# Kernel tuning notes

Hardware: AMD Instinct MI355X
Metric: run time of the kernel (lower is better)

The kernel has to match this reference:

```python
import jax, jax.numpy as jnp
import numpy as np

BETA1 = 0.9
BETA2 = 0.8
THRESH = 1.0  # snntorch Leaky default threshold

T, B, NI, NH, NO = 100, 1024, 256, 512, 10


def setup_inputs() -> dict:
    key = jax.random.key(0)
    kx, k1, k2 = jax.random.split(key, 3)
    x = jax.random.normal(kx, (T, B, NI), dtype=jnp.float32)
    # Weight_synapse 'bin_random_prob' init: binary {0, w} with given probs
    W1 = (jax.random.uniform(k1, (NH, NI)) < 0.8).astype(jnp.float32) * 0.5
    W2 = (jax.random.uniform(k2, (NO, NH)) < 0.5).astype(jnp.float32) * 0.5
    return {"x": x, "W1": W1, "W2": W2}


def _lif(mem, cur, beta):
    # snntorch Leaky, reset_mechanism='subtract': reset from previous mem,
    # then mem = beta*mem + cur - reset*threshold; spk = heaviside(mem - thr)
    reset = (mem > THRESH).astype(cur.dtype)
    mem = beta * mem + cur - reset * THRESH
    spk = (mem > THRESH).astype(cur.dtype)
    return spk, mem


def reference(x, W1, W2):
    b = x.shape[1]
    mem1_0 = jnp.zeros((b, W1.shape[0]), x.dtype)
    mem2_0 = jnp.zeros((b, W2.shape[0]), x.dtype)

    def step(carry, xt):
        mem1, mem2 = carry
        cur1 = xt @ W1.T                      # [B, NH]
        spk1, mem1 = _lif(mem1, cur1, BETA1)
        cur2 = spk1 @ W2.T                    # [B, NO]
        spk2, mem2 = _lif(mem2, cur2, BETA2)
        return (mem1, mem2), (cur1, cur2, spk1, spk2, mem1, mem2)

    _, (cur1, cur2, spk1, spk2, mem1, mem2) = jax.lax.scan(step, (mem1_0, mem2_0), x)
    # matches {'cur':[c1,c2],'spks':[s1,s2],'mem':[m1,m2]}, each stacked on time
    return cur1, cur2, spk1, spk2, mem1, mem2
```

## Files before the change

kernel.cpp:

```cpp
#include <hip/hip_runtime.h>

#define TT 100
#define BB 1024
#define NI 256
#define NH 512
#define NO 10
#define TB (TT*BB)
#define GK 512
#define GN 512

constexpr long long C1_OFF = 0;
constexpr long long C2_OFF = 52428800LL;
constexpr long long S1_OFF = 53452800LL;
constexpr long long S2_OFF = 105881600LL;
constexpr long long M1_OFF = 106905600LL;
constexpr long long M2_OFF = 159334400LL;

typedef short bf16x8 __attribute__((ext_vector_type(8)));
typedef float f32x4 __attribute__((ext_vector_type(4)));

__device__ __forceinline__ unsigned int rne_bf16(float f) {
    unsigned int u = __float_as_uint(f);
    return (u + 0x7fffu + ((u >> 16) & 1u)) >> 16;
}

__device__ __forceinline__ unsigned int pack_hilo(float f) {
    unsigned int hi = rne_bf16(f);
    float hif = __uint_as_float(hi << 16);
    float e = f - hif;
    unsigned int lo = rne_bf16(e);
    return (hi & 0xffffu) | (lo << 16);
}

__global__ void prep_w_kernel(const float* __restrict__ W1, short* __restrict__ Wp) {
    int i = blockIdx.x * blockDim.x + threadIdx.x;
    if (i >= NH * NI / 4) return;
    float4 v = ((const float4*)W1)[i];
    float f[4] = {v.x, v.y, v.z, v.w};
    uint4 o;
    unsigned int* op = &o.x;
    #pragma unroll
    for (int j = 0; j < 4; ++j) {
        unsigned int hb = __float_as_uint(f[j]) >> 16;
        op[j] = hb | (hb << 16);
    }
    ((uint4*)Wp)[i] = o;
}

__launch_bounds__(256, 2)
__global__ void gemm1_kernel(const float* __restrict__ x, const short* __restrict__ Wp,
                             float* __restrict__ C) {
    __shared__ short As[128][40];
    __shared__ short Ws[128][40];
    const int tid = threadIdx.x;
    const int bid = blockIdx.x;
    const int m0 = (bid >> 2) * 128;
    const int n0 = (bid & 3) * 128;
    const int wid = tid >> 6;
    const int lane = tid & 63;
    const int wm = (wid >> 1) * 64;
    const int wn = (wid & 1) * 64;

    f32x4 acc[4][4] = {};

    const int srow = tid >> 2;
    const int sc4 = tid & 3;
    const long long ax0 = (long long)(m0 + srow) * NI + sc4 * 4;
    const long long ax1 = ax0 + 64LL * NI;
    const long long wr0 = (long long)(n0 + srow) * GK + sc4 * 8;
    const long long wr1 = wr0 + 64LL * GK;

    const int fr = lane & 15;
    const int fk = (lane >> 4) * 8;

    float4 a0 = *(const float4*)&x[ax0];
    float4 a1 = *(const float4*)&x[ax1];
    uint4 w0 = *(const uint4*)&Wp[wr0];
    uint4 w1 = *(const uint4*)&Wp[wr1];
    uint4 pa0, pa1;
    pa0.x = pack_hilo(a0.x); pa0.y = pack_hilo(a0.y); pa0.z = pack_hilo(a0.z); pa0.w = pack_hilo(a0.w);
    pa1.x = pack_hilo(a1.x); pa1.y = pack_hilo(a1.y); pa1.z = pack_hilo(a1.z); pa1.w = pack_hilo(a1.w);

    for (int kt = 0; kt < GK / 32; ++kt) {
        __syncthreads();
        *(uint4*)&As[srow][sc4 * 8]      = pa0;
        *(uint4*)&As[srow + 64][sc4 * 8] = pa1;
        *(uint4*)&Ws[srow][sc4 * 8]      = w0;
        *(uint4*)&Ws[srow + 64][sc4 * 8] = w1;
        __syncthreads();

        const int ktn = (kt + 1 < GK / 32) ? kt + 1 : kt;
        a0 = *(const float4*)&x[ax0 + (long long)ktn * 16];
        a1 = *(const float4*)&x[ax1 + (long long)ktn * 16];
        w0 = *(const uint4*)&Wp[wr0 + (long long)ktn * 32];
        w1 = *(const uint4*)&Wp[wr1 + (long long)ktn * 32];
        pa0.x = pack_hilo(a0.x); pa0.y = pack_hilo(a0.y); pa0.z = pack_hilo(a0.z); pa0.w = pack_hilo(a0.w);
        pa1.x = pack_hilo(a1.x); pa1.y = pack_hilo(a1.y); pa1.z = pack_hilo(a1.z); pa1.w = pack_hilo(a1.w);

        bf16x8 af[4], wf[4];
        #pragma unroll
        for (int i = 0; i < 4; ++i) {
            af[i] = *(const bf16x8*)&As[wm + i * 16 + fr][fk];
            wf[i] = *(const bf16x8*)&Ws[wn + i * 16 + fr][fk];
        }
        #pragma unroll
        for (int i = 0; i < 4; ++i)
            #pragma unroll
            for (int j = 0; j < 4; ++j)
                acc[i][j] = __builtin_amdgcn_mfma_f32_16x16x32_bf16(af[i], wf[j], acc[i][j], 0, 0, 0);
    }

    const int col = lane & 15;
    const int rbase = (lane >> 4) * 4;
    #pragma unroll
    for (int i = 0; i < 4; ++i) {
        #pragma unroll
        for (int j = 0; j < 4; ++j) {
            long long base = (long long)(m0 + wm + i * 16 + rbase) * GN + (n0 + wn + j * 16 + col);
            #pragma unroll
            for (int r = 0; r < 4; ++r)
                C[base + (long long)r * GN] = acc[i][j][r];
        }
    }
}

__launch_bounds__(512)
__global__ void lif_kernel(const float* __restrict__ cur1, const float* __restrict__ W2,
                           float* __restrict__ out) {
    const int b = blockIdx.x;
    const int h = threadIdx.x;
    const int w = h >> 6;
    const int lane = h & 63;

    __shared__ unsigned long long wmks[2][8];
    __shared__ unsigned long long w2ms[NO][8];

    #pragma unroll
    for (int o = 0; o < NO; ++o) {
        unsigned long long mk = __ballot(W2[o * NH + h] != 0.0f);
        if (lane == 0) w2ms[o][w] = mk;
    }
    __syncthreads();
    unsigned long long w2m[8];
    if (h < NO) {
        #pragma unroll
        for (int i = 0; i < 8; ++i) w2m[i] = w2ms[h][i];
    }

    float m1 = 0.0f, m2 = 0.0f;
    const long long idx1 = (long long)b * NH + h;
    const float* c1p = cur1 + idx1;
    float* s1p = out + S1_OFF + idx1;
    float* m1p = out + M1_OFF + idx1;
    const long long st1 = (long long)BB * NH;

    for (int t = 0; t < TT; ++t) {
        float c1 = c1p[(long long)t * st1];
        float rst = (m1 > 1.0f) ? 1.0f : 0.0f;
        m1 = 0.9f * m1 + c1 - rst;
        float s1 = (m1 > 1.0f) ? 1.0f : 0.0f;
        s1p[(long long)t * st1] = s1;
        m1p[(long long)t * st1] = m1;

        unsigned long long mk = __ballot(s1 != 0.0f);
        if (lane == 0) wmks[t & 1][w] = mk;
        __syncthreads();

        if (h < NO) {
            int cnt = 0;
            #pragma unroll
            for (int i = 0; i < 8; ++i) cnt += __popcll(wmks[t & 1][i] & w2m[i]);
            float c2 = 0.5f * (float)cnt;
            float rst2 = (m2 > 1.0f) ? 1.0f : 0.0f;
            m2 = 0.8f * m2 + c2 - rst2;
            float s2 = (m2 > 1.0f) ? 1.0f : 0.0f;
            long long o2 = (long long)t * (BB * NO) + b * NO + h;
            out[C2_OFF + o2] = c2;
            out[S2_OFF + o2] = s2;
            out[M2_OFF + o2] = m2;
        }
    }
}

extern "C" void kernel_launch(void* const* d_in, const int* in_sizes, int n_in,
                              void* d_out, int out_size, void* d_ws, size_t ws_size,
                              hipStream_t stream) {
    const float* x  = (const float*)d_in[0];
    const float* W1 = (const float*)d_in[1];
    const float* W2 = (const float*)d_in[2];
    float* out = (float*)d_out;

    short* Wp = (short*)(out + S1_OFF);
    float* C1 = out + C1_OFF;

    {
        int w4 = NH * NI / 4;
        prep_w_kernel<<<(w4 + 255) / 256, 256, 0, stream>>>(W1, Wp);
    }
    {
        gemm1_kernel<<<(TB / 128) * (GN / 128), 256, 0, stream>>>(x, Wp, C1);
    }
    lif_kernel<<<BB, NH, 0, stream>>>(C1, W2, out);
}
```

Before: 261.8 us.

## Chunk time into two GEMM+LIF passes, async LDS weight loads with swizzled pre-tiled layout

Splits the time axis into two chunks so each gemm1 launch writes a smaller cur1 slab that the following lif pass reads while it may still be cache-resident. The LIF state is carried between chunks by reading back the last stored mem values. W1 is pre-tiled into a swizzled image and streamed into a double-buffered LDS tile with global_load_lds, removing register staging and bank conflicts. The LIF loop also prefetches the next cur1 value. This adds launches and a serial dependency between chunks, and it relocates the weight scratch inside the output buffer.

```diff
diff --git a/kernel.cpp b/kernel.cpp
--- a/kernel.cpp
+++ b/kernel.cpp
@@ -8,6 +8,7 @@
 #define TB (TT*BB)
 #define GK 512
 #define GN 512
+#define TCH 50
 
 constexpr long long C1_OFF = 0;
 constexpr long long C2_OFF = 52428800LL;
@@ -32,11 +33,27 @@
     return (hi & 0xffffu) | (lo << 16);
 }
 
-__global__ void prep_w_kernel(const float* __restrict__ W1, short* __restrict__ Wp) {
+__device__ __forceinline__ void pack4(uint4& d, const float4& a) {
+    d.x = pack_hilo(a.x); d.y = pack_hilo(a.y); d.z = pack_hilo(a.z); d.w = pack_hilo(a.w);
+}
+
+__device__ __forceinline__ void gload16(const void* g, void* l) {
+    __builtin_amdgcn_global_load_lds(
+        (const __attribute__((address_space(1))) void*)g,
+        (__attribute__((address_space(3))) void*)l, 16, 0, 0);
+}
+
+__global__ void prep_w_kernel(const float* __restrict__ W1, short* __restrict__ Wimg) {
     int i = blockIdx.x * blockDim.x + threadIdx.x;
-    if (i >= NH * NI / 4) return;
-    float4 v = ((const float4*)W1)[i];
-    float f[4] = {v.x, v.y, v.z, v.w};
+    if (i >= 4 * 16 * 128 * 4) return;
+    int c16 = i & 3;
+    int r   = (i >> 2) & 127;
+    int kt  = (i >> 9) & 15;
+    int p   = i >> 13;
+    int usrc = c16 ^ ((r >> 1) & 3);
+    int kbase = kt * 16 + usrc * 4;
+    float4 w = *(const float4*)&W1[(long long)(p * 128 + r) * NI + kbase];
+    float f[4] = {w.x, w.y, w.z, w.w};
     uint4 o;
     unsigned int* op = &o.x;
     #pragma unroll
@@ -44,18 +61,19 @@
         unsigned int hb = __float_as_uint(f[j]) >> 16;
         op[j] = hb | (hb << 16);
     }
-    ((uint4*)Wp)[i] = o;
+    ((uint4*)Wimg)[i] = o;
 }
 
 __launch_bounds__(256, 2)
-__global__ void gemm1_kernel(const float* __restrict__ x, const short* __restrict__ Wp,
+__global__ void gemm1_kernel(const float* __restrict__ x, const short* __restrict__ Wimg,
                              float* __restrict__ C) {
     __shared__ short As[128][40];
-    __shared__ short Ws[128][40];
+    __shared__ short Ws[2][128][32];
     const int tid = threadIdx.x;
     const int bid = blockIdx.x;
     const int m0 = (bid >> 2) * 128;
-    const int n0 = (bid & 3) * 128;
+    const int p  = bid & 3;
+    const int n0 = p * 128;
     const int wid = tid >> 6;
     const int lane = tid & 63;
     const int wm = (wid >> 1) * 64;
@@ -67,47 +85,51 @@
     const int sc4 = tid & 3;
     const long long ax0 = (long long)(m0 + srow) * NI + sc4 * 4;
     const long long ax1 = ax0 + 64LL * NI;
-    const long long wr0 = (long long)(n0 + srow) * GK + sc4 * 8;
-    const long long wr1 = wr0 + 64LL * GK;
 
     const int fr = lane & 15;
     const int fk = (lane >> 4) * 8;
+    const int swz = (((lane >> 4) ^ ((fr >> 1) & 3)) << 4);
+
+    const short* wbase = Wimg + (long long)p * 16 * 4096;
+    const int c0 = wid * 2;
+
+    gload16(wbase + (c0    ) * 512 + lane * 8, (char*)&Ws[0][0][0] + (c0    ) * 1024);
+    gload16(wbase + (c0 + 1) * 512 + lane * 8, (char*)&Ws[0][0][0] + (c0 + 1) * 1024);
 
     float4 a0 = *(const float4*)&x[ax0];
     float4 a1 = *(const float4*)&x[ax1];
-    uint4 w0 = *(const uint4*)&Wp[wr0];
-    uint4 w1 = *(const uint4*)&Wp[wr1];
     uint4 pa0, pa1;
-    pa0.x = pack_hilo(a0.x); pa0.y = pack_hilo(a0.y); pa0.z = pack_hilo(a0.z); pa0.w = pack_hilo(a0.w);
-    pa1.x = pack_hilo(a1.x); pa1.y = pack_hilo(a1.y); pa1.z = pack_hilo(a1.z); pa1.w = pack_hilo(a1.w);
-
+    pack4(pa0, a0); pack4(pa1, a1);
+
+    int buf = 0;
     for (int kt = 0; kt < GK / 32; ++kt) {
         __syncthreads();
         *(uint4*)&As[srow][sc4 * 8]      = pa0;
         *(uint4*)&As[srow + 64][sc4 * 8] = pa1;
-        *(uint4*)&Ws[srow][sc4 * 8]      = w0;
-        *(uint4*)&Ws[srow + 64][sc4 * 8] = w1;
         __syncthreads();
 
-        const int ktn = (kt + 1 < GK / 32) ? kt + 1 : kt;
-        a0 = *(const float4*)&x[ax0 + (long long)ktn * 16];
-        a1 = *(const float4*)&x[ax1 + (long long)ktn * 16];
-        w0 = *(const uint4*)&Wp[wr0 + (long long)ktn * 32];
-        w1 = *(const uint4*)&Wp[wr1 + (long long)ktn * 32];
-        pa0.x = pack_hilo(a0.x); pa0.y = pack_hilo(a0.y); pa0.z = pack_hilo(a0.z); pa0.w = pack_hilo(a0.w);
-        pa1.x = pack_hilo(a1.x); pa1.y = pack_hilo(a1.y); pa1.z = pack_hilo(a1.z); pa1.w = pack_hilo(a1.w);
+        if (kt + 1 < GK / 32) {
+            const short* wt = wbase + (kt + 1) * 4096;
+            gload16(wt + (c0    ) * 512 + lane * 8, (char*)&Ws[buf ^ 1][0][0] + (c0    ) * 1024);
+            gload16(wt + (c0 + 1) * 512 + lane * 8, (char*)&Ws[buf ^ 1][0][0] + (c0 + 1) * 1024);
+            a0 = *(const float4*)&x[ax0 + (long long)(kt + 1) * 16];
+            a1 = *(const float4*)&x[ax1 + (long long)(kt + 1) * 16];
+        }
 
         bf16x8 af[4], wf[4];
         #pragma unroll
         for (int i = 0; i < 4; ++i) {
             af[i] = *(const bf16x8*)&As[wm + i * 16 + fr][fk];
-            wf[i] = *(const bf16x8*)&Ws[wn + i * 16 + fr][fk];
+            wf[i] = *(const bf16x8*)((const char*)&Ws[buf][wn + i * 16 + fr][0] + swz);
         }
         #pragma unroll
         for (int i = 0; i < 4; ++i)
             #pragma unroll
             for (int j = 0; j < 4; ++j)
                 acc[i][j] = __builtin_amdgcn_mfma_f32_16x16x32_bf16(af[i], wf[j], acc[i][j], 0, 0, 0);
+
+        if (kt + 1 < GK / 32) { pack4(pa0, a0); pack4(pa1, a1); }
+        buf ^= 1;
     }
 
     const int col = lane & 15;
@@ -126,7 +148,7 @@
 
 __launch_bounds__(512)
 __global__ void lif_kernel(const float* __restrict__ cur1, const float* __restrict__ W2,
-                           float* __restrict__ out) {
+                           float* __restrict__ out, int t0) {
     const int b = blockIdx.x;
     const int h = threadIdx.x;
     const int w = h >> 6;
@@ -147,15 +169,23 @@
         for (int i = 0; i < 8; ++i) w2m[i] = w2ms[h][i];
     }
 
-    float m1 = 0.0f, m2 = 0.0f;
     const long long idx1 = (long long)b * NH + h;
     const float* c1p = cur1 + idx1;
     float* s1p = out + S1_OFF + idx1;
     float* m1p = out + M1_OFF + idx1;
     const long long st1 = (long long)BB * NH;
 
-    for (int t = 0; t < TT; ++t) {
-        float c1 = c1p[(long long)t * st1];
+    float m1 = 0.0f, m2 = 0.0f;
+    if (t0 != 0) {
+        m1 = m1p[(long long)(t0 - 1) * st1];
+        if (h < NO) m2 = out[M2_OFF + (long long)(t0 - 1) * (BB * NO) + b * NO + h];
+    }
+
+    float c1 = c1p[(long long)t0 * st1];
+    for (int t = t0; t < t0 + TCH; ++t) {
+        float c1n = 0.0f;
+        if (t + 1 < t0 + TCH) c1n = c1p[(long long)(t + 1) * st1];
+
         float rst = (m1 > 1.0f) ? 1.0f : 0.0f;
         m1 = 0.9f * m1 + c1 - rst;
         float s1 = (m1 > 1.0f) ? 1.0f : 0.0f;
@@ -179,6 +209,7 @@
             out[S2_OFF + o2] = s2;
             out[M2_OFF + o2] = m2;
         }
+        c1 = c1n;
     }
 }
 
@@ -190,15 +221,17 @@
     const float* W2 = (const float*)d_in[2];
     float* out = (float*)d_out;
 
-    short* Wp = (short*)(out + S1_OFF);
+    short* Wp = (short*)(out + S1_OFF + (long long)TCH * BB * NH);
     float* C1 = out + C1_OFF;
 
     {
-        int w4 = NH * NI / 4;
-        prep_w_kernel<<<(w4 + 255) / 256, 256, 0, stream>>>(W1, Wp);
-    }
-    {
-        gemm1_kernel<<<(TB / 128) * (GN / 128), 256, 0, stream>>>(x, Wp, C1);
-    }
-    lif_kernel<<<BB, NH, 0, stream>>>(C1, W2, out);
-}
+        int units = NH * GK / 8;
+        prep_w_kernel<<<(units + 255) / 256, 256, 0, stream>>>(W1, Wp);
+    }
+    for (int c = 0; c < TT / TCH; ++c) {
+        const int t0 = c * TCH;
+        gemm1_kernel<<<(TCH * BB / 128) * (GN / 128), 256, 0, stream>>>(
+            x + (long long)t0 * BB * NI, Wp, C1 + (long long)t0 * BB * GN);
+        lif_kernel<<<BB, NH, 0, stream>>>(C1, W2, out, t0);
+    }
+}
```

Result: slower. 299.7 us (+14.5%).

## Fuse layer-1 GEMM with LIF recurrence and atomically accumulate layer-2 current

Applied to the files above, without the earlier changes.

Replaces the separate GEMM and LIF kernels with one persistent kernel. Each block keeps a 64-column slice of W1 in LDS and walks time for a 32-row batch group, computing cur1 with MFMA, updating mem1 in registers and writing cur1, spk1 and mem1 directly. This removes the round trip of cur1 through global memory. The spike bitmasks are popcounted against W2 masks and atomically added into cur2, and a small final kernel runs the layer-2 LIF scan. In exchange it runs only 256 blocks with a sync per timestep, needs an extra zeroing pass, and adds float atomics.

```diff
diff --git a/kernel.cpp b/kernel.cpp
--- a/kernel.cpp
+++ b/kernel.cpp
@@ -5,9 +5,7 @@
 #define NI 256
 #define NH 512
 #define NO 10
-#define TB (TT*BB)
 #define GK 512
-#define GN 512
 
 constexpr long long C1_OFF = 0;
 constexpr long long C2_OFF = 52428800LL;
@@ -30,6 +28,10 @@
     float e = f - hif;
     unsigned int lo = rne_bf16(e);
     return (hi & 0xffffu) | (lo << 16);
+}
+
+__device__ __forceinline__ void pack4(uint4& d, const float4& a) {
+    d.x = pack_hilo(a.x); d.y = pack_hilo(a.y); d.z = pack_hilo(a.z); d.w = pack_hilo(a.w);
 }
 
 __global__ void prep_w_kernel(const float* __restrict__ W1, short* __restrict__ Wp) {
@@ -47,137 +49,149 @@
     ((uint4*)Wp)[i] = o;
 }
 
-__launch_bounds__(256, 2)
-__global__ void gemm1_kernel(const float* __restrict__ x, const short* __restrict__ Wp,
-                             float* __restrict__ C) {
-    __shared__ short As[128][40];
-    __shared__ short Ws[128][40];
+__global__ void zero_c2_kernel(float* __restrict__ c2) {
+    int i = blockIdx.x * blockDim.x + threadIdx.x;
+    if (i < TT * BB * NO / 4) ((float4*)c2)[i] = float4{0.f, 0.f, 0.f, 0.f};
+}
+
+__launch_bounds__(512, 1)
+__global__ void fused_kernel(const float* __restrict__ x, const short* __restrict__ Wp,
+                             const float* __restrict__ W2, float* __restrict__ out) {
+    __shared__ short Wl[64][512];
+    __shared__ short Al[2][32][512];
+    __shared__ unsigned long long bal[2][8][4];
+    __shared__ unsigned long long w2m_lds[NO];
+
     const int tid = threadIdx.x;
     const int bid = blockIdx.x;
-    const int m0 = (bid >> 2) * 128;
-    const int n0 = (bid & 3) * 128;
+    const int xcd = bid & 7;
+    const int j8  = bid >> 3;
+    const int bgrp = xcd * 4 + (j8 >> 3);
+    const int nc   = j8 & 7;
+    const int b0 = bgrp * 32;
+    const int n0 = nc * 64;
+
     const int wid = tid >> 6;
     const int lane = tid & 63;
-    const int wm = (wid >> 1) * 64;
-    const int wn = (wid & 1) * 64;
-
-    f32x4 acc[4][4] = {};
-
-    const int srow = tid >> 2;
-    const int sc4 = tid & 3;
-    const long long ax0 = (long long)(m0 + srow) * NI + sc4 * 4;
-    const long long ax1 = ax0 + 64LL * NI;
-    const long long wr0 = (long long)(n0 + srow) * GK + sc4 * 8;
-    const long long wr1 = wr0 + 64LL * GK;
-
+    const int mw = wid >> 2;
+    const int nw = wid & 3;
     const int fr = lane & 15;
-    const int fk = (lane >> 4) * 8;
-
-    float4 a0 = *(const float4*)&x[ax0];
-    float4 a1 = *(const float4*)&x[ax1];
-    uint4 w0 = *(const uint4*)&Wp[wr0];
-    uint4 w1 = *(const uint4*)&Wp[wr1];
-    uint4 pa0, pa1;
-    pa0.x = pack_hilo(a0.x); pa0.y = pack_hilo(a0.y); pa0.z = pack_hilo(a0.z); pa0.w = pack_hilo(a0.w);
-    pa1.x = pack_hilo(a1.x); pa1.y = pack_hilo(a1.y); pa1.z = pack_hilo(a1.z); pa1.w = pack_hilo(a1.w);
-
-    for (int kt = 0; kt < GK / 32; ++kt) {
+    const int g  = lane >> 4;
+    const int mrow = mw * 16 + fr;
+    const int nrow = nw * 16 + fr;
+
+    if (wid == 0) {
+        #pragma unroll
+        for (int o = 0; o < NO; ++o)
+            w2m_lds[o] = __ballot(W2[o * NH + n0 + lane] != 0.0f);
+    }
+    #pragma unroll
+    for (int u8 = 0; u8 < 8; ++u8) {
+        int e = u8 * 512 + tid;
+        int r = e >> 6, u = e & 63;
+        uint4 v = ((const uint4*)Wp)[(long long)n0 * 64 + e];
+        *(uint4*)&Wl[r][((u ^ (r & 7)) * 8)] = v;
+    }
+    const int arow = tid >> 4;
+    const int au0 = (tid & 15) * 4;
+    {
+        const float* xs = x + ((long long)b0 + arow) * NI;
+        #pragma unroll
+        for (int uu = 0; uu < 4; ++uu) {
+            float4 a = *(const float4*)&xs[(au0 + uu) * 4];
+            uint4 pa; pack4(pa, a);
+            *(uint4*)&Al[0][arow][(((au0 + uu) ^ (arow & 7)) * 8)] = pa;
+        }
+    }
+    float4 rawOdd[4], rawEven[4];
+    #pragma unroll
+    for (int uu = 0; uu < 4; ++uu) {
+        rawOdd[uu]  = *(const float4*)&x[((long long)1 * BB + b0 + arow) * NI + (au0 + uu) * 4];
+        rawEven[uu] = *(const float4*)&x[((long long)2 * BB + b0 + arow) * NI + (au0 + uu) * 4];
+    }
+    __syncthreads();
+    unsigned long long w2m_reg = (tid < 32 * NO) ? w2m_lds[tid >> 5] : 0ULL;
+
+    float m1v[4] = {0.f, 0.f, 0.f, 0.f};
+
+    auto step = [&](int T, float4 (&RAW)[4]) {
+        f32x4 a = {0.f, 0.f, 0.f, 0.f};
+        #pragma unroll
+        for (int kt = 0; kt < 16; ++kt) {
+            bf16x8 af = *(const bf16x8*)&Al[T & 1][mrow][(((kt * 4 + g) ^ (fr & 7)) * 8)];
+            bf16x8 wf = *(const bf16x8*)&Wl[nrow][(((kt * 4 + g) ^ (fr & 7)) * 8)];
+            a = __builtin_amdgcn_mfma_f32_16x16x32_bf16(af, wf, a, 0, 0, 0);
+        }
+        float s1v[4];
+        #pragma unroll
+        for (int r = 0; r < 4; ++r) {
+            float c1 = a[r];
+            float rst = (m1v[r] > 1.0f) ? 1.0f : 0.0f;
+            m1v[r] = 0.9f * m1v[r] + c1 - rst;
+            s1v[r] = (m1v[r] > 1.0f) ? 1.0f : 0.0f;
+            long long ob = ((long long)T * BB + b0 + mw * 16 + g * 4 + r) * NH + n0 + nw * 16 + fr;
+            out[C1_OFF + ob] = c1;
+            out[S1_OFF + ob] = s1v[r];
+            out[M1_OFF + ob] = m1v[r];
+        }
+        #pragma unroll
+        for (int r = 0; r < 4; ++r) {
+            unsigned long long bm = __ballot(s1v[r] != 0.0f);
+            if (lane == 0) bal[T & 1][wid][r] = bm;
+        }
+        if (T + 1 < TT) {
+            #pragma unroll
+            for (int uu = 0; uu < 4; ++uu) {
+                uint4 pa; pack4(pa, RAW[uu]);
+                *(uint4*)&Al[(T + 1) & 1][arow][(((au0 + uu) ^ (arow & 7)) * 8)] = pa;
+            }
+            int tl = (T + 3 < TT) ? T + 3 : TT - 1;
+            #pragma unroll
+            for (int uu = 0; uu < 4; ++uu)
+                RAW[uu] = *(const float4*)&x[((long long)tl * BB + b0 + arow) * NI + (au0 + uu) * 4];
+        }
         __syncthreads();
-        *(uint4*)&As[srow][sc4 * 8]      = pa0;
-        *(uint4*)&As[srow + 64][sc4 * 8] = pa1;
-        *(uint4*)&Ws[srow][sc4 * 8]      = w0;
-        *(uint4*)&Ws[srow + 64][sc4 * 8] = w1;
-        __syncthreads();
-
-        const int ktn = (kt + 1 < GK / 32) ? kt + 1 : kt;
-        a0 = *(const float4*)&x[ax0 + (long long)ktn * 16];
-        a1 = *(const float4*)&x[ax1 + (long long)ktn * 16];
-        w0 = *(const uint4*)&Wp[wr0 + (long long)ktn * 32];
-        w1 = *(const uint4*)&Wp[wr1 + (long long)ktn * 32];
-        pa0.x = pack_hilo(a0.x); pa0.y = pack_hilo(a0.y); pa0.z = pack_hilo(a0.z); pa0.w = pack_hilo(a0.w);
-        pa1.x = pack_hilo(a1.x); pa1.y = pack_hilo(a1.y); pa1.z = pack_hilo(a1.z); pa1.w = pack_hilo(a1.w);
-
-        bf16x8 af[4], wf[4];
-        #pragma unroll
-        for (int i = 0; i < 4; ++i) {
-            af[i] = *(const bf16x8*)&As[wm + i * 16 + fr][fk];
-            wf[i] = *(const bf16x8*)&Ws[wn + i * 16 + fr][fk];
-        }
-        #pragma unroll
-        for (int i = 0; i < 4; ++i)
+        if (tid < 32 * NO) {
+            int r = tid & 31, o = tid >> 5;
+            int mwr = r >> 4, l15 = r & 15;
+            unsigned long long row64 = 0;
             #pragma unroll
-            for (int j = 0; j < 4; ++j)
-                acc[i][j] = __builtin_amdgcn_mfma_f32_16x16x32_bf16(af[i], wf[j], acc[i][j], 0, 0, 0);
-    }
-
-    const int col = lane & 15;
-    const int rbase = (lane >> 4) * 4;
-    #pragma unroll
-    for (int i = 0; i < 4; ++i) {
-        #pragma unroll
-        for (int j = 0; j < 4; ++j) {
-            long long base = (long long)(m0 + wm + i * 16 + rbase) * GN + (n0 + wn + j * 16 + col);
-            #pragma unroll
-            for (int r = 0; r < 4; ++r)
-                C[base + (long long)r * GN] = acc[i][j][r];
-        }
+            for (int nwx = 0; nwx < 4; ++nwx)
+                row64 |= ((bal[T & 1][mwr * 4 + nwx][l15 & 3] >> ((l15 >> 2) * 16)) & 0xFFFFULL)
+                         << (16 * nwx);
+            int cnt = __popcll(row64 & w2m_reg);
+            atomicAdd(out + C2_OFF + ((long long)T * BB + b0 + r) * NO + o, 0.5f * (float)cnt);
+        }
+    };
+
+    for (int tp = 0; tp < TT; tp += 2) {
+        step(tp,     rawOdd);
+        step(tp + 1, rawEven);
     }
 }
 
 __launch_bounds__(512)
-__global__ void lif_kernel(const float* __restrict__ cur1, const float* __restrict__ W2,
-                           float* __restrict__ out) {
-    const int b = blockIdx.x;
-    const int h = threadIdx.x;
-    const int w = h >> 6;
-    const int lane = h & 63;
-
-    __shared__ unsigned long long wmks[2][8];
-    __shared__ unsigned long long w2ms[NO][8];
-
-    #pragma unroll
-    for (int o = 0; o < NO; ++o) {
-        unsigned long long mk = __ballot(W2[o * NH + h] != 0.0f);
-        if (lane == 0) w2ms[o][w] = mk;
-    }
-    __syncthreads();
-    unsigned long long w2m[8];
-    if (h < NO) {
-        #pragma unroll
-        for (int i = 0; i < 8; ++i) w2m[i] = w2ms[h][i];
-    }
-
-    float m1 = 0.0f, m2 = 0.0f;
-    const long long idx1 = (long long)b * NH + h;
-    const float* c1p = cur1 + idx1;
-    float* s1p = out + S1_OFF + idx1;
-    float* m1p = out + M1_OFF + idx1;
-    const long long st1 = (long long)BB * NH;
-
-    for (int t = 0; t < TT; ++t) {
-        float c1 = c1p[(long long)t * st1];
-        float rst = (m1 > 1.0f) ? 1.0f : 0.0f;
-        m1 = 0.9f * m1 + c1 - rst;
-        float s1 = (m1 > 1.0f) ? 1.0f : 0.0f;
-        s1p[(long long)t * st1] = s1;
-        m1p[(long long)t * st1] = m1;
-
-        unsigned long long mk = __ballot(s1 != 0.0f);
-        if (lane == 0) wmks[t & 1][w] = mk;
-        __syncthreads();
-
-        if (h < NO) {
-            int cnt = 0;
-            #pragma unroll
-            for (int i = 0; i < 8; ++i) cnt += __popcll(wmks[t & 1][i] & w2m[i]);
-            float c2 = 0.5f * (float)cnt;
-            float rst2 = (m2 > 1.0f) ? 1.0f : 0.0f;
-            m2 = 0.8f * m2 + c2 - rst2;
+__global__ void lif2_kernel(float* __restrict__ out) {
+    int j = blockIdx.x * 512 + threadIdx.x;
+    if (j >= BB * NO) return;
+    const float* c2p = out + C2_OFF + j;
+    float* s2p = out + S2_OFF + j;
+    float* m2p = out + M2_OFF + j;
+    const int st = BB * NO;
+    float m2 = 0.f;
+    float v[4];
+    #pragma unroll
+    for (int k = 0; k < 4; ++k) v[k] = c2p[(long long)k * st];
+    for (int t = 0; t < TT; t += 4) {
+        #pragma unroll
+        for (int k = 0; k < 4; ++k) {
+            float c2 = v[k];
+            if (t + 4 + k < TT) v[k] = c2p[(long long)(t + 4 + k) * st];
+            float rst = (m2 > 1.0f) ? 1.0f : 0.0f;
+            m2 = 0.8f * m2 + c2 - rst;
             float s2 = (m2 > 1.0f) ? 1.0f : 0.0f;
-            long long o2 = (long long)t * (BB * NO) + b * NO + h;
-            out[C2_OFF + o2] = c2;
-            out[S2_OFF + o2] = s2;
-            out[M2_OFF + o2] = m2;
+            s2p[(long long)(t + k) * st] = s2;
+            m2p[(long long)(t + k) * st] = m2;
         }
     }
 }
@@ -190,15 +204,10 @@
     const float* W2 = (const float*)d_in[2];
     float* out = (float*)d_out;
 
-    short* Wp = (short*)(out + S1_OFF);
-    float* C1 = out + C1_OFF;
-
-    {
-        int w4 = NH * NI / 4;
-        prep_w_kernel<<<(w4 + 255) / 256, 256, 0, stream>>>(W1, Wp);
-    }
-    {
-        gemm1_kernel<<<(TB / 128) * (GN / 128), 256, 0, stream>>>(x, Wp, C1);
-    }
-    lif_kernel<<<BB, NH, 0, stream>>>(C1, W2, out);
-}
+    short* Wp = (short*)(out + S2_OFF);
+
+    prep_w_kernel<<<(NH * NI / 4 + 255) / 256, 256, 0, stream>>>(W1, Wp);
+    zero_c2_kernel<<<(TT * BB * NO / 4 + 255) / 256, 256, 0, stream>>>(out + C2_OFF);
+    fused_kernel<<<256, 512, 0, stream>>>(x, Wp, W2, out);
+    lif2_kernel<<<(BB * NO + 511) / 512, 512, 0, stream>>>(out);
+}
```

Result: slower. 354.3 us (+35.4%).
